# Performance work log

Measured on AMD Instinct MI355X. Metric: run time of the kernel, lower is better.

The kernel has to match this reference:

```python
import jax, jax.numpy as jnp
import numpy as np
from jax import lax

GRID_N = 80
C_FEAT = 128
HID = 256
NLAYERS = 12


def _make_grid_mesh(n):
    xs = np.linspace(-0.9, 0.9, n, dtype=np.float32)
    X, Y = np.meshgrid(xs, xs, indexing='xy')
    verts = np.stack([X.ravel(), Y.ravel(), np.zeros(n * n, np.float32)], 1)
    idx = np.arange(n * n).reshape(n, n)
    a = idx[:-1, :-1].ravel(); b = idx[:-1, 1:].ravel()
    c = idx[1:, :-1].ravel(); d = idx[1:, 1:].ravel()
    faces = np.concatenate([np.stack([a, b, c], 1), np.stack([b, d, c], 1)], 0)
    return verts, faces.astype(np.int64)


def _edges_and_inv(faces):
    F = faces.shape[0]
    e = np.concatenate([faces[:, [0, 1]], faces[:, [1, 2]], faces[:, [2, 0]]], 0)
    e = np.sort(e, 1)
    edges, inv = np.unique(e, axis=0, return_inverse=True)
    inv = inv.reshape(-1)
    return edges.astype(np.int32), inv[:F], inv[F:2 * F], inv[2 * F:]


def _subdivide_faces(faces, V):
    # new vertex k is midpoint of unique edge k, placed at index V + k
    edges, i01, i12, i20 = _edges_and_inv(faces)
    m01 = V + i01; m12 = V + i12; m20 = V + i20
    v0, v1, v2 = faces[:, 0], faces[:, 1], faces[:, 2]
    nf = np.concatenate([np.stack([v0, m01, m20], 1), np.stack([v1, m12, m01], 1),
                         np.stack([v2, m20, m12], 1), np.stack([m01, m12, m20], 1)], 0)
    return edges, nf


def _topology():
    verts0, f1 = _make_grid_mesh(GRID_N)
    V1 = verts0.shape[0]
    edges1, f2 = _subdivide_faces(f1, V1)
    V2 = V1 + edges1.shape[0]
    edges2, f3 = _subdivide_faces(f2, V2)
    V3 = V2 + edges2.shape[0]
    edges3 = _edges_and_inv(f3)[0]
    return verts0, edges1, edges2, edges3, V3


def _vert_align(feat, verts):
    # feat [C,H,W]; sample bilinearly at vertex (x,y) in [-1,1], align_corners, zero padding
    C, H, W = feat.shape
    fx = (verts[:, 0] + 1.0) * 0.5 * (W - 1)
    fy = (verts[:, 1] + 1.0) * 0.5 * (H - 1)
    x0 = jnp.floor(fx); y0 = jnp.floor(fy)
    wx = fx - x0; wy = fy - y0
    x0i = x0.astype(jnp.int32); y0i = y0.astype(jnp.int32)
    fT = jnp.transpose(feat, (1, 2, 0))  # [H,W,C]

    def samp(yi, xi):
        valid = ((yi >= 0) & (yi < H) & (xi >= 0) & (xi < W)).astype(feat.dtype)
        v = fT[jnp.clip(yi, 0, H - 1), jnp.clip(xi, 0, W - 1)]
        return v * valid[:, None]

    return (samp(y0i, x0i) * ((1 - wy) * (1 - wx))[:, None]
            + samp(y0i, x0i + 1) * ((1 - wy) * wx)[:, None]
            + samp(y0i + 1, x0i) * (wy * (1 - wx))[:, None]
            + samp(y0i + 1, x0i + 1) * (wy * wx)[:, None])


def _gconv(x, e0, e1, w, b):
    # pytorch3d GraphConv: w0(x) + sum_{j in N(i)} w1(x_j), undirected edges
    h0 = x @ w[0] + b[0]
    h1 = x @ w[1] + b[1]
    agg = jnp.zeros_like(h0).at[e0].add(h1[e1]).at[e1].add(h1[e0])
    return h0 + agg


def _stage(feat, edges, w_in, b_in, w_h, b_h, w_out, b_out):
    e0, e1 = edges[:, 0], edges[:, 1]
    x = _gconv(feat, e0, e1, w_in, b_in)

    def body(xc, p):
        return _gconv(xc, e0, e1, p[0], p[1]), None

    x, _ = lax.scan(body, x, (w_h, b_h))
    coords = _gconv(x, e0, e1, w_out, b_out)
    return x, coords


def _subdiv(f, edges):
    # SubdivideMeshes feature/vertex rule: append edge midpoints
    return jnp.concatenate([f, 0.5 * (f[edges[:, 0]] + f[edges[:, 1]])], 0)


def setup_inputs() -> dict:
    key = jax.random.key(0)
    ks = jax.random.split(key, 16)
    verts0, edges1, edges2, edges3, V3 = _topology()

    def pw(k, din, dout, L=None):
        shape = (L, 2, din, dout) if L else (2, din, dout)
        return jax.random.normal(k, shape, dtype=jnp.float32) / np.float32(np.sqrt(7.0 * din))

    din2 = C_FEAT + HID
    inp = {
        'conv64': jax.random.normal(ks[0], (C_FEAT, 56, 56), jnp.float32),
        'conv128': jax.random.normal(ks[1], (C_FEAT, 28, 28), jnp.float32),
        'conv256': jax.random.normal(ks[2], (C_FEAT, 14, 14), jnp.float32),
        'verts0': jnp.asarray(verts0),
        'edges1': jnp.asarray(edges1), 'edges2': jnp.asarray(edges2), 'edges3': jnp.asarray(edges3),
        'w_in1': pw(ks[3], C_FEAT, HID), 'b_in1': jnp.zeros((2, HID), jnp.float32),
        'w_h1': pw(ks[4], HID, HID, NLAYERS), 'b_h1': jnp.zeros((NLAYERS, 2, HID), jnp.float32),
        'w_out1': pw(ks[5], HID, 3), 'b_out1': jnp.zeros((2, 3), jnp.float32),
        'w_in2': pw(ks[6], din2, HID), 'b_in2': jnp.zeros((2, HID), jnp.float32),
        'w_h2': pw(ks[7], HID, HID, NLAYERS), 'b_h2': jnp.zeros((NLAYERS, 2, HID), jnp.float32),
        'w_out2': pw(ks[8], HID, 3), 'b_out2': jnp.zeros((2, 3), jnp.float32),
        'w_in3': pw(ks[9], din2, HID), 'b_in3': jnp.zeros((2, HID), jnp.float32),
        'w_h3': pw(ks[10], HID, HID, NLAYERS), 'b_h3': jnp.zeros((NLAYERS, 2, HID), jnp.float32),
        'w_out3': pw(ks[11], HID, 3), 'b_out3': jnp.zeros((2, 3), jnp.float32),
    }
    return inp


def reference(conv64, conv128, conv256, verts0,
              w_in1, b_in1, w_h1, b_h1, w_out1, b_out1,
              w_in2, b_in2, w_h2, b_h2, w_out2, b_out2,
              w_in3, b_in3, w_h3, b_h3, w_out3, b_out3,
              edges1, edges2, edges3):
    # stage 1: vert_align on conv64 + 14 graph convs -> coords
    x, c1 = _stage(_vert_align(conv64, verts0), edges1, w_in1, b_in1, w_h1, b_h1, w_out1, b_out1)
    v2 = _subdiv(c1, edges1)
    h2 = _subdiv(x, edges1)
    f2 = jnp.concatenate([_vert_align(conv128, v2), h2], 1)
    x, c2 = _stage(f2, edges2, w_in2, b_in2, w_h2, b_h2, w_out2, b_out2)
    v3 = _subdiv(c2, edges2)
    h3 = _subdiv(x, edges2)
    f3 = jnp.concatenate([_vert_align(conv256, v3), h3], 1)
    _, c3 = _stage(f3, edges3, w_in3, b_in3, w_h3, b_h3, w_out3, b_out3)
    return c3
```

## Files before the change

### kernel.cpp

```cpp
#include <hip/hip_runtime.h>
#include <utility>

#define HID 256

typedef __attribute__((ext_vector_type(8))) short bf16x8;
typedef __attribute__((ext_vector_type(4))) float f32x4;
typedef __attribute__((ext_vector_type(4))) unsigned short us4;
typedef __attribute__((ext_vector_type(8))) unsigned short us8;

constexpr size_t MAXN3 = 100489;
constexpr size_t MAXE3 = 300200;

constexpr size_t OFF_IN1 = 0;
constexpr size_t OFF_IN2 = OFF_IN1 + 2 * 256 * 128;
constexpr size_t OFF_IN3 = OFF_IN2 + 2 * 256 * 384;
constexpr size_t OFF_H1  = OFF_IN3 + 2 * 256 * 384;
constexpr size_t OFF_H2  = OFF_H1 + 24 * 256 * 256;
constexpr size_t OFF_H3  = OFF_H2 + 24 * 256 * 256;
constexpr size_t WT_TOTAL = OFF_H3 + 24 * 256 * 256;

__device__ __attribute__((aligned(16))) unsigned short g_Ah[MAXN3 * 256];
__device__ __attribute__((aligned(16))) unsigned short g_Al[MAXN3 * 256];
__device__ __attribute__((aligned(16))) unsigned short g_Bh[MAXN3 * 256];
__device__ __attribute__((aligned(16))) unsigned short g_Bl[MAXN3 * 256];
__device__ __attribute__((aligned(16))) unsigned short g_Gh[MAXN3 * 256];
__device__ __attribute__((aligned(16))) unsigned short g_Gl[MAXN3 * 256];
__device__ __attribute__((aligned(16))) unsigned short g_Dh[MAXN3 * 256];
__device__ __attribute__((aligned(16))) unsigned short g_Dl[MAXN3 * 256];
__device__ __attribute__((aligned(16))) unsigned short g_VAh[MAXN3 * 128];
__device__ __attribute__((aligned(16))) unsigned short g_VAl[MAXN3 * 128];
__device__ float g_C0[MAXN3 * 3];
__device__ float g_C2[MAXN3 * 3];
__device__ float g_Vv[MAXN3 * 3];
__device__ float g_T [56 * 56 * 128];
__device__ __attribute__((aligned(16))) unsigned short g_Wth[WT_TOTAL];
__device__ __attribute__((aligned(16))) unsigned short g_Wtl[WT_TOTAL];
__device__ int g_deg   [MAXN3];
__device__ int g_rowptr[MAXN3 + 1];
__device__ int g_cursor[MAXN3];
__device__ int g_adj   [2 * MAXE3];
__device__ int g_bsum  [128];

__device__ inline float b2f(unsigned short h) {
  return __uint_as_float((unsigned)h << 16);
}
__device__ inline void fsplit(float f, unsigned short& h, unsigned short& l) {
  unsigned u = __float_as_uint(f);
  h = (unsigned short)(u >> 16);
  float hf = __uint_as_float(u & 0xffff0000u);
  l = (unsigned short)(__float_as_uint(f - hf) >> 16);
}

#define GLOAD16(g, l)                                                       \
  __builtin_amdgcn_global_load_lds(                                        \
      (const __attribute__((address_space(1))) unsigned*)(const void*)(g), \
      (__attribute__((address_space(3))) unsigned*)(void*)(l), 16, 0, 0)

__global__ __launch_bounds__(256) void k_wtrans(const float* __restrict__ W,
                                                unsigned short* __restrict__ Oh,
                                                unsigned short* __restrict__ Ol,
                                                int K) {
  __shared__ float Ls[64][65];
  int ktb = blockIdx.x, cb = blockIdx.y, mat = blockIdx.z;
  int nktb = gridDim.x;
  const float* Wm = W + (size_t)mat * K * 256;
  int t = threadIdx.x;
#pragma unroll
  for (int i = 0; i < 16; ++i) {
    int idx = i * 256 + t;
    int kk = idx >> 6, cc = idx & 63;
    Ls[kk][cc] = Wm[(size_t)(ktb * 64 + kk) * 256 + cb * 64 + cc];
  }
  __syncthreads();
  size_t tb = ((size_t)(mat * 4 + cb) * nktb + ktb) * 4096;
#pragma unroll
  for (int i = 0; i < 2; ++i) {
    int c = t * 2 + i;
    int n = c >> 3, sp = c & 7;
    int kbase = (sp ^ (n & 7)) * 8;
    unsigned short hb[8], lb[8];
#pragma unroll
    for (int j = 0; j < 8; ++j) {
      float v = Ls[kbase + j][n];
      unsigned short hi, lo;
      fsplit(v, hi, lo);
      hb[j] = hi;
      lb[j] = lo;
    }
    *(us4*)(Oh + tb + c * 8)     = (us4){hb[0], hb[1], hb[2], hb[3]};
    *(us4*)(Oh + tb + c * 8 + 4) = (us4){hb[4], hb[5], hb[6], hb[7]};
    *(us4*)(Ol + tb + c * 8)     = (us4){lb[0], lb[1], lb[2], lb[3]};
    *(us4*)(Ol + tb + c * 8 + 4) = (us4){lb[4], lb[5], lb[6], lb[7]};
  }
}


__global__ __launch_bounds__(256) void k_count(const int* __restrict__ edges,
                                               int* __restrict__ deg, int E) {
  int e = blockIdx.x * blockDim.x + threadIdx.x;
  if (e >= E) return;
  atomicAdd(&deg[edges[2 * e + 0]], 1);
  atomicAdd(&deg[edges[2 * e + 1]], 1);
}

__global__ __launch_bounds__(256) void k_scan_part(const int* __restrict__ deg,
                                                   int* __restrict__ bsum, int N) {
  __shared__ int s[256];
  int t = threadIdx.x;
  int base = blockIdx.x * 1024 + t * 4;
  int v = 0;
#pragma unroll
  for (int i = 0; i < 4; ++i) {
    int idx = base + i;
    if (idx < N) v += deg[idx];
  }
  s[t] = v;
  __syncthreads();
  for (int off = 128; off > 0; off >>= 1) {
    if (t < off) s[t] += s[t + off];
    __syncthreads();
  }
  if (t == 0) bsum[blockIdx.x] = s[0];
}

__global__ __launch_bounds__(128) void k_scan_top(int* __restrict__ bsum, int nb) {
  __shared__ int s[128];
  int t = threadIdx.x;
  s[t] = (t < nb) ? bsum[t] : 0;
  __syncthreads();
  for (int off = 1; off < 128; off <<= 1) {
    int v = (t >= off) ? s[t - off] : 0;
    __syncthreads();
    s[t] += v;
    __syncthreads();
  }
  if (t < nb) bsum[t] = (t == 0) ? 0 : s[t - 1];
}

__global__ __launch_bounds__(256) void k_scan_write(const int* __restrict__ deg,
                                                    const int* __restrict__ bsum,
                                                    int* __restrict__ rowptr,
                                                    int* __restrict__ cursor, int N) {
  __shared__ int s[256];
  int t = threadIdx.x;
  int base = blockIdx.x * 1024;
  int d[4];
  int local = 0;
#pragma unroll
  for (int i = 0; i < 4; ++i) {
    int idx = base + t * 4 + i;
    d[i] = (idx < N) ? deg[idx] : 0;
    local += d[i];
  }
  s[t] = local;
  __syncthreads();
  for (int off = 1; off < 256; off <<= 1) {
    int v = (t >= off) ? s[t - off] : 0;
    __syncthreads();
    s[t] += v;
    __syncthreads();
  }
  int run = bsum[blockIdx.x] + s[t] - local;
#pragma unroll
  for (int i = 0; i < 4; ++i) {
    int idx = base + t * 4 + i;
    if (idx < N) {
      rowptr[idx] = run;
      cursor[idx] = run;
    }
    run += d[i];
  }
  if (blockIdx.x == gridDim.x - 1 && t == 255) rowptr[N] = run;
}

__global__ __launch_bounds__(256) void k_fill(const int* __restrict__ edges,
                                              int* __restrict__ cursor,
                                              int* __restrict__ adj, int E) {
  int e = blockIdx.x * blockDim.x + threadIdx.x;
  if (e >= E) return;
  int a = edges[2 * e + 0];
  int b = edges[2 * e + 1];
  adj[atomicAdd(&cursor[a], 1)] = b;
  adj[atomicAdd(&cursor[b], 1)] = a;
}


__global__ __launch_bounds__(128) void k_transpose(const float* __restrict__ in,
                                                   float* __restrict__ out, int HW) {
  int p = blockIdx.x;
  int c = threadIdx.x;
  if (p < HW) out[(size_t)p * 128 + c] = in[(size_t)c * HW + p];
}

__global__ __launch_bounds__(128) void k_vert_align(const float* __restrict__ fT,
                                                    const float* __restrict__ verts,
                                                    unsigned short* __restrict__ oh,
                                                    unsigned short* __restrict__ ol,
                                                    int N, int H, int W) {
  int v = blockIdx.x;
  if (v >= N) return;
  int c = threadIdx.x;
  float vx = verts[(size_t)v * 3 + 0];
  float vy = verts[(size_t)v * 3 + 1];
  float fx = (vx + 1.f) * 0.5f * (float)(W - 1);
  float fy = (vy + 1.f) * 0.5f * (float)(H - 1);
  float x0f = floorf(fx), y0f = floorf(fy);
  float wx = fx - x0f, wy = fy - y0f;
  int x0 = (int)x0f, y0 = (int)y0f;
  float acc = 0.f;
#pragma unroll
  for (int dy = 0; dy < 2; ++dy) {
#pragma unroll
    for (int dx = 0; dx < 2; ++dx) {
      int yi = y0 + dy, xi = x0 + dx;
      bool valid = (yi >= 0) && (yi < H) && (xi >= 0) && (xi < W);
      int yc = min(max(yi, 0), H - 1);
      int xc = min(max(xi, 0), W - 1);
      float val = fT[((size_t)yc * W + xc) * 128 + c];
      float wgt = (dy ? wy : 1.f - wy) * (dx ? wx : 1.f - wx);
      acc += valid ? val * wgt : 0.f;
    }
  }
  unsigned short h, l;
  fsplit(acc, h, l);
  oh[(size_t)v * 128 + c] = h;
  ol[(size_t)v * 128 + c] = l;
}

template <int CH>
__global__ __launch_bounds__(256) void k_gather(const int* __restrict__ rowptr,
                                                const int* __restrict__ adj,
                                                const unsigned short* __restrict__ Xh,
                                                const unsigned short* __restrict__ Xl,
                                                unsigned short* __restrict__ Gh,
                                                unsigned short* __restrict__ Gl, int N) {
  constexpr int TPV = CH / 8;
  int idx = blockIdx.x * blockDim.x + threadIdx.x;
  int v = idx / TPV;
  if (v >= N) return;
  int c = (idx % TPV) * 8;
  float a[8] = {};
  int lo = rowptr[v], hi = rowptr[v + 1];
  for (int i = lo; i < hi; ++i) {
    size_t base = (size_t)adj[i] * CH + c;
    us8 h = *(const us8*)(Xh + base);
    us8 l = *(const us8*)(Xl + base);
#pragma unroll
    for (int j = 0; j < 8; ++j) a[j] += b2f(h[j]) + b2f(l[j]);
  }
  us8 oh, ol;
#pragma unroll
  for (int j = 0; j < 8; ++j) {
    unsigned short hh, ll;
    fsplit(a[j], hh, ll);
    oh[j] = hh;
    ol[j] = ll;
  }
  *(us8*)(Gh + (size_t)v * CH + c) = oh;
  *(us8*)(Gl + (size_t)v * CH + c) = ol;
}

struct Panels {
  const unsigned short* ph[4];
  const unsigned short* pl[4];
  int ks[4];
  int ld[4];
};

#define SWZ(row, slot) (((row) * 64) + (((slot) ^ ((row) & 7)) << 3))

__global__ __launch_bounds__(256) void k_layer(
    Panels pd, int Kmm,
    const unsigned short* __restrict__ w0h, const unsigned short* __restrict__ w0l,
    const unsigned short* __restrict__ w1h, const unsigned short* __restrict__ w1l,
    int Kw,
    const float* __restrict__ b0, const float* __restrict__ b1,
    const int* __restrict__ deg,
    unsigned short* __restrict__ Yh, unsigned short* __restrict__ Yl, int N) {
  __shared__ __attribute__((aligned(16))) unsigned short Xh_lds[128 * 64];
  __shared__ __attribute__((aligned(16))) unsigned short Xl_lds[128 * 64];
  __shared__ __attribute__((aligned(16))) unsigned short Wh_lds[4096];
  __shared__ __attribute__((aligned(16))) unsigned short Wl_lds[4096];
  int tid = threadIdx.x;
  int lane = tid & 63;
  int wid = tid >> 6;
  int wm = wid & 1, wn = wid >> 1;

  int nrt = (N + 127) >> 7;
  int total = nrt * 4;
  int flat = blockIdx.x;
  int rowtile, colblk;
  if ((flat & ~31) + 32 <= total) {
    int sub = flat & 31;
    rowtile = (flat >> 5) * 8 + (sub & 7);
    colblk = sub >> 3;
  } else {
    rowtile = flat >> 2;
    colblk = flat & 3;
  }
  int row0 = rowtile * 128;
  int col0 = colblk * 64;
  int nktbw = Kw >> 6;

  f32x4 acc[4][2];
#pragma unroll
  for (int m = 0; m < 4; ++m)
#pragma unroll
    for (int n = 0; n < 2; ++n) acc[m][n] = (f32x4){0.f, 0.f, 0.f, 0.f};

  for (int kt = 0; kt < Kmm; kt += 64) {
    int pi = (kt >= pd.ks[1]) + (kt >= pd.ks[2]) + (kt >= pd.ks[3]);
    const unsigned short* bph = pd.ph[pi];
    const unsigned short* bpl = pd.pl[pi];
    int ld = pd.ld[pi];
    int koff = kt - pd.ks[pi];
#pragma unroll
    for (int i = 0; i < 4; ++i) {
      int c = (wid * 4 + i) * 64 + lane;
      int row = c >> 3, slot = c & 7;
      int vg = min(row0 + row, N - 1);
      size_t srcoff = (size_t)vg * ld + koff + ((slot ^ (row & 7)) << 3);
      GLOAD16(bph + srcoff, &Xh_lds[(size_t)c * 8]);
      GLOAD16(bpl + srcoff, &Xl_lds[(size_t)c * 8]);
    }
    const unsigned short* th;
    const unsigned short* tl;
    {
      int ktb = (kt < Kw) ? (kt >> 6) : ((kt - Kw) >> 6);
      const unsigned short* mh = (kt < Kw) ? w0h : w1h;
      const unsigned short* ml = (kt < Kw) ? w0l : w1l;
      size_t tb = ((size_t)(colblk * nktbw + ktb)) * 4096;
      th = mh + tb;
      tl = ml + tb;
    }
#pragma unroll
    for (int i = 0; i < 2; ++i) {
      int inst = wid * 2 + i;
      GLOAD16(th + inst * 512 + lane * 8, &Wh_lds[inst * 512]);
      GLOAD16(tl + inst * 512 + lane * 8, &Wl_lds[inst * 512]);
    }
    __syncthreads();
#pragma unroll
    for (int ks = 0; ks < 2; ++ks) {
      int slot = ks * 4 + (lane >> 4);
      bf16x8 ah[4], al[4];
#pragma unroll
      for (int m = 0; m < 4; ++m) {
        int row = wm * 64 + m * 16 + (lane & 15);
        int off = SWZ(row, slot);
        ah[m] = *(const bf16x8*)&Xh_lds[off];
        al[m] = *(const bf16x8*)&Xl_lds[off];
      }
      bf16x8 bh[2], bl[2];
#pragma unroll
      for (int n = 0; n < 2; ++n) {
        int nr = wn * 32 + n * 16 + (lane & 15);
        int wi = SWZ(nr, slot);
        bh[n] = *(const bf16x8*)&Wh_lds[wi];
        bl[n] = *(const bf16x8*)&Wl_lds[wi];
      }
#pragma unroll
      for (int m = 0; m < 4; ++m)
#pragma unroll
        for (int n = 0; n < 2; ++n) {
          f32x4 c = acc[m][n];
          c = __builtin_amdgcn_mfma_f32_16x16x32_bf16(al[m], bh[n], c, 0, 0, 0);
          c = __builtin_amdgcn_mfma_f32_16x16x32_bf16(ah[m], bl[n], c, 0, 0, 0);
          c = __builtin_amdgcn_mfma_f32_16x16x32_bf16(ah[m], bh[n], c, 0, 0, 0);
          acc[m][n] = c;
        }
    }
    __syncthreads();
  }

#pragma unroll
  for (int m = 0; m < 4; ++m) {
    int rbase = row0 + wm * 64 + m * 16 + (lane >> 4) * 4;
    float dv[4];
#pragma unroll
    for (int r = 0; r < 4; ++r)
      dv[r] = (rbase + r < N) ? (float)deg[rbase + r] : 0.f;
#pragma unroll
    for (int n = 0; n < 2; ++n) {
      int col = col0 + wn * 32 + n * 16 + (lane & 15);
      float bb0 = b0[col], bb1 = b1[col];
      f32x4 v = acc[m][n];
#pragma unroll
      for (int r = 0; r < 4; ++r) {
        int row = rbase + r;
        if (row < N) {
          unsigned short h, l;
          fsplit(v[r] + bb0 + dv[r] * bb1, h, l);
          Yh[(size_t)row * HID + col] = h;
          Yl[(size_t)row * HID + col] = l;
        }
      }
    }
  }
}

__global__ __launch_bounds__(256) void k_rowdot6(const unsigned short* __restrict__ Xh,
                                                 const unsigned short* __restrict__ Xl,
                                                 const float* __restrict__ W,
                                                 const float* __restrict__ b,
                                                 float* __restrict__ Y0,
                                                 float* __restrict__ Y1, int N) {
  int gid = blockIdx.x * blockDim.x + threadIdx.x;
  int row = gid >> 6;
  int lane = threadIdx.x & 63;
  if (row >= N) return;
  size_t base = (size_t)row * HID + lane * 4;
  us4 hv = *(const us4*)(Xh + base);
  us4 lv = *(const us4*)(Xl + base);
  float s[6] = {0.f, 0.f, 0.f, 0.f, 0.f, 0.f};
#pragma unroll
  for (int k = 0; k < 4; ++k) {
    float x = b2f(hv[k]) + b2f(lv[k]);
    int kk = lane * 4 + k;
#pragma unroll
    for (int j = 0; j < 3; ++j) {
      s[j]     += x * W[kk * 3 + j];
      s[3 + j] += x * W[768 + kk * 3 + j];
    }
  }
#pragma unroll
  for (int off = 32; off > 0; off >>= 1)
#pragma unroll
    for (int j = 0; j < 6; ++j) s[j] += __shfl_down(s[j], off);
  if (lane == 0) {
#pragma unroll
    for (int j = 0; j < 3; ++j) {
      Y0[(size_t)row * 3 + j] = s[j] + b[j];
      Y1[(size_t)row * 3 + j] = s[3 + j] + b[3 + j];
    }
  }
}

__global__ __launch_bounds__(256) void k_scatter3(const int* __restrict__ edges,
                                                  const float* __restrict__ H,
                                                  float* __restrict__ OUT, int E) {
  int e = blockIdx.x * blockDim.x + threadIdx.x;
  if (e >= E) return;
  int a = edges[(size_t)e * 2 + 0];
  int b = edges[(size_t)e * 2 + 1];
#pragma unroll
  for (int k = 0; k < 3; ++k) {
    atomicAdd(&OUT[(size_t)a * 3 + k], H[(size_t)b * 3 + k]);
    atomicAdd(&OUT[(size_t)b * 3 + k], H[(size_t)a * 3 + k]);
  }
}

__global__ __launch_bounds__(256) void k_subdiv3(const float* __restrict__ c,
                                                 const int* __restrict__ edges,
                                                 float* __restrict__ v, int N, int E) {
  int i = blockIdx.x * blockDim.x + threadIdx.x;
  if (i >= N + E) return;
  if (i < N) {
#pragma unroll
    for (int k = 0; k < 3; ++k) v[(size_t)i * 3 + k] = c[(size_t)i * 3 + k];
  } else {
    int e = i - N;
    int a = edges[(size_t)e * 2 + 0];
    int b = edges[(size_t)e * 2 + 1];
#pragma unroll
    for (int k = 0; k < 3; ++k)
      v[(size_t)i * 3 + k] = 0.5f * (c[(size_t)a * 3 + k] + c[(size_t)b * 3 + k]);
  }
}

__global__ __launch_bounds__(256) void k_subdiv_feat(const unsigned short* __restrict__ xh,
                                                     const unsigned short* __restrict__ xl,
                                                     const int* __restrict__ edges,
                                                     unsigned short* __restrict__ oh,
                                                     unsigned short* __restrict__ ol,
                                                     int N, int E) {
  int idx = blockIdx.x * blockDim.x + threadIdx.x;
  int v = idx >> 5;
  if (v >= N + E) return;
  int c = (idx & 31) * 8;
  us8 rh, rl;
  if (v < N) {
    rh = *(const us8*)(xh + (size_t)v * HID + c);
    rl = *(const us8*)(xl + (size_t)v * HID + c);
  } else {
    int e = v - N;
    int a = edges[(size_t)e * 2 + 0];
    int b = edges[(size_t)e * 2 + 1];
    us8 ahv = *(const us8*)(xh + (size_t)a * HID + c);
    us8 alv = *(const us8*)(xl + (size_t)a * HID + c);
    us8 bhv = *(const us8*)(xh + (size_t)b * HID + c);
    us8 blv = *(const us8*)(xl + (size_t)b * HID + c);
#pragma unroll
    for (int j = 0; j < 8; ++j) {
      float f = 0.5f * ((b2f(ahv[j]) + b2f(alv[j])) + (b2f(bhv[j]) + b2f(blv[j])));
      unsigned short hh, ll;
      fsplit(f, hh, ll);
      rh[j] = hh;
      rl[j] = ll;
    }
  }
  *(us8*)(oh + (size_t)v * HID + c) = rh;
  *(us8*)(ol + (size_t)v * HID + c) = rl;
}


extern "C" void kernel_launch(void* const* d_in, const int* in_sizes, int n_in,
                              void* d_out, int out_size, void* d_ws, size_t ws_size,
                              hipStream_t stream) {
  const float* conv64  = (const float*)d_in[0];
  const float* conv128 = (const float*)d_in[1];
  const float* conv256 = (const float*)d_in[2];
  const float* verts0  = (const float*)d_in[3];
  const int*   edges1  = (const int*)d_in[4];
  const int*   edges2  = (const int*)d_in[5];
  const int*   edges3  = (const int*)d_in[6];
  const float* w_in1 = (const float*)d_in[7],  *b_in1 = (const float*)d_in[8];
  const float* w_h1  = (const float*)d_in[9],  *b_h1  = (const float*)d_in[10];
  const float* w_out1= (const float*)d_in[11], *b_out1= (const float*)d_in[12];
  const float* w_in2 = (const float*)d_in[13], *b_in2 = (const float*)d_in[14];
  const float* w_h2  = (const float*)d_in[15], *b_h2  = (const float*)d_in[16];
  const float* w_out2= (const float*)d_in[17], *b_out2= (const float*)d_in[18];
  const float* w_in3 = (const float*)d_in[19], *b_in3 = (const float*)d_in[20];
  const float* w_h3  = (const float*)d_in[21], *b_h3  = (const float*)d_in[22];
  const float* w_out3= (const float*)d_in[23], *b_out3= (const float*)d_in[24];

  const int N1 = in_sizes[3] / 3;
  const int E1 = in_sizes[4] / 2;
  const int E2 = in_sizes[5] / 2;
  const int E3 = in_sizes[6] / 2;
  const int N2 = N1 + E1;
  const int N3 = N2 + E2;
  if ((size_t)N3 > MAXN3 || (size_t)E3 > MAXE3) return;

  unsigned short *Ah, *Al, *Bh, *Bl, *Gh, *Gl, *Dh, *Dl, *VAh, *VAl;
  float *C0, *C2, *Vv, *T;
  unsigned short *Wth, *Wtl;
  int *deg, *rowptr, *cursor, *adj, *bsum;
  hipGetSymbolAddress((void**)&Ah,  HIP_SYMBOL(g_Ah));
  hipGetSymbolAddress((void**)&Al,  HIP_SYMBOL(g_Al));
  hipGetSymbolAddress((void**)&Bh,  HIP_SYMBOL(g_Bh));
  hipGetSymbolAddress((void**)&Bl,  HIP_SYMBOL(g_Bl));
  hipGetSymbolAddress((void**)&Gh,  HIP_SYMBOL(g_Gh));
  hipGetSymbolAddress((void**)&Gl,  HIP_SYMBOL(g_Gl));
  hipGetSymbolAddress((void**)&Dh,  HIP_SYMBOL(g_Dh));
  hipGetSymbolAddress((void**)&Dl,  HIP_SYMBOL(g_Dl));
  hipGetSymbolAddress((void**)&VAh, HIP_SYMBOL(g_VAh));
  hipGetSymbolAddress((void**)&VAl, HIP_SYMBOL(g_VAl));
  hipGetSymbolAddress((void**)&C0, HIP_SYMBOL(g_C0));
  hipGetSymbolAddress((void**)&C2, HIP_SYMBOL(g_C2));
  hipGetSymbolAddress((void**)&Vv, HIP_SYMBOL(g_Vv));
  hipGetSymbolAddress((void**)&T,  HIP_SYMBOL(g_T));
  hipGetSymbolAddress((void**)&Wth, HIP_SYMBOL(g_Wth));
  hipGetSymbolAddress((void**)&Wtl, HIP_SYMBOL(g_Wtl));
  hipGetSymbolAddress((void**)&deg,    HIP_SYMBOL(g_deg));
  hipGetSymbolAddress((void**)&rowptr, HIP_SYMBOL(g_rowptr));
  hipGetSymbolAddress((void**)&cursor, HIP_SYMBOL(g_cursor));
  hipGetSymbolAddress((void**)&adj,    HIP_SYMBOL(g_adj));
  hipGetSymbolAddress((void**)&bsum,   HIP_SYMBOL(g_bsum));

  k_wtrans<<<dim3(2, 4, 2),  256, 0, stream>>>(w_in1, Wth + OFF_IN1, Wtl + OFF_IN1, 128);
  k_wtrans<<<dim3(6, 4, 2),  256, 0, stream>>>(w_in2, Wth + OFF_IN2, Wtl + OFF_IN2, 384);
  k_wtrans<<<dim3(6, 4, 2),  256, 0, stream>>>(w_in3, Wth + OFF_IN3, Wtl + OFF_IN3, 384);
  k_wtrans<<<dim3(4, 4, 24), 256, 0, stream>>>(w_h1,  Wth + OFF_H1,  Wtl + OFF_H1,  256);
  k_wtrans<<<dim3(4, 4, 24), 256, 0, stream>>>(w_h2,  Wth + OFF_H2,  Wtl + OFF_H2,  256);
  k_wtrans<<<dim3(4, 4, 24), 256, 0, stream>>>(w_h3,  Wth + OFF_H3,  Wtl + OFF_H3,  256);

  const int BIG = 0x7fffffff;

  auto layerGrid = [](int N) { return dim3((unsigned)(((N + 127) / 128) * 4)); };

  auto build_csr = [&](const int* edges, int E, int N) {
    hipMemsetAsync(deg, 0, (size_t)N * sizeof(int), stream);
    k_count<<<(E + 255) / 256, 256, 0, stream>>>(edges, deg, E);
    int nb = (N + 1023) / 1024;
    k_scan_part<<<nb, 256, 0, stream>>>(deg, bsum, N);
    k_scan_top<<<1, 128, 0, stream>>>(bsum, nb);
    k_scan_write<<<nb, 256, 0, stream>>>(deg, bsum, rowptr, cursor, N);
    k_fill<<<(E + 255) / 256, 256, 0, stream>>>(edges, cursor, adj, E);
  };

  auto gconv_hidden = [&](size_t offH, const float* bh, int N) {
    unsigned short *Xh = Ah, *Xl = Al, *Yh = Bh, *Yl = Bl;
    for (int l = 0; l < 12; ++l) {
      const unsigned short* w0h = Wth + offH + (size_t)(2 * l + 0) * 65536;
      const unsigned short* w0l = Wtl + offH + (size_t)(2 * l + 0) * 65536;
      const unsigned short* w1h = Wth + offH + (size_t)(2 * l + 1) * 65536;
      const unsigned short* w1l = Wtl + offH + (size_t)(2 * l + 1) * 65536;
      const float* b0 = bh + (size_t)l * 2 * HID;
      const float* b1 = b0 + HID;
      k_gather<256><<<((size_t)N * 32 + 255) / 256, 256, 0, stream>>>(
          rowptr, adj, Xh, Xl, Gh, Gl, N);
      Panels pd = {{Xh, Gh, nullptr, nullptr}, {Xl, Gl, nullptr, nullptr},
                   {0, 256, BIG, BIG}, {256, 256, 0, 0}};
      k_layer<<<layerGrid(N), 256, 0, stream>>>(pd, 512, w0h, w0l, w1h, w1l, 256,
                                                b0, b1, deg, Yh, Yl, N);
      std::swap(Xh, Yh);
      std::swap(Xl, Yl);
    }
  };

  auto gconv_out = [&](const unsigned short* Xh, const unsigned short* Xl,
                       const float* wo, const float* bo,
                       float* Cdst, const int* edges, int E, int N) {
    k_rowdot6<<<((size_t)N * 64 + 255) / 256, 256, 0, stream>>>(Xh, Xl, wo, bo, Cdst, C2, N);
    k_scatter3<<<(E + 255) / 256, 256, 0, stream>>>(edges, C2, Cdst, E);
  };

  build_csr(edges1, E1, N1);
  k_transpose<<<56 * 56, 128, 0, stream>>>(conv64, T, 56 * 56);
  k_vert_align<<<N1, 128, 0, stream>>>(T, verts0, VAh, VAl, N1, 56, 56);
  k_gather<128><<<((size_t)N1 * 16 + 255) / 256, 256, 0, stream>>>(
      rowptr, adj, VAh, VAl, Gh, Gl, N1);
  {
    Panels pd = {{VAh, Gh, nullptr, nullptr}, {VAl, Gl, nullptr, nullptr},
                 {0, 128, BIG, BIG}, {128, 128, 0, 0}};
    k_layer<<<layerGrid(N1), 256, 0, stream>>>(pd, 256,
        Wth + OFF_IN1, Wtl + OFF_IN1, Wth + OFF_IN1 + 32768, Wtl + OFF_IN1 + 32768, 128,
        b_in1, b_in1 + HID, deg, Ah, Al, N1);
  }
  gconv_hidden(OFF_H1, b_h1, N1);
  gconv_out(Ah, Al, w_out1, b_out1, C0, edges1, E1, N1);
  k_subdiv3<<<(N2 + 255) / 256, 256, 0, stream>>>(C0, edges1, Vv, N1, E1);
  k_subdiv_feat<<<((size_t)N2 * 32 + 255) / 256, 256, 0, stream>>>(
      Ah, Al, edges1, Dh, Dl, N1, E1);

  build_csr(edges2, E2, N2);
  k_transpose<<<28 * 28, 128, 0, stream>>>(conv128, T, 28 * 28);
  k_vert_align<<<N2, 128, 0, stream>>>(T, Vv, VAh, VAl, N2, 28, 28);
  k_gather<128><<<((size_t)N2 * 16 + 255) / 256, 256, 0, stream>>>(
      rowptr, adj, VAh, VAl, Gh, Gl, N2);
  k_gather<256><<<((size_t)N2 * 32 + 255) / 256, 256, 0, stream>>>(
      rowptr, adj, Dh, Dl, Bh, Bl, N2);
  {
    const size_t m0 = OFF_IN2, m1 = OFF_IN2 + (size_t)256 * 384;
    Panels pd = {{VAh, Dh, Gh, Bh}, {VAl, Dl, Gl, Bl},
                 {0, 128, 384, 512}, {128, 256, 128, 256}};
    k_layer<<<layerGrid(N2), 256, 0, stream>>>(pd, 768,
        Wth + m0, Wtl + m0, Wth + m1, Wtl + m1, 384,
        b_in2, b_in2 + HID, deg, Ah, Al, N2);
  }
  gconv_hidden(OFF_H2, b_h2, N2);
  gconv_out(Ah, Al, w_out2, b_out2, C0, edges2, E2, N2);
  k_subdiv3<<<(N3 + 255) / 256, 256, 0, stream>>>(C0, edges2, Vv, N2, E2);
  k_subdiv_feat<<<((size_t)N3 * 32 + 255) / 256, 256, 0, stream>>>(
      Ah, Al, edges2, Dh, Dl, N2, E2);

  build_csr(edges3, E3, N3);
  k_transpose<<<14 * 14, 128, 0, stream>>>(conv256, T, 14 * 14);
  k_vert_align<<<N3, 128, 0, stream>>>(T, Vv, VAh, VAl, N3, 14, 14);
  k_gather<128><<<((size_t)N3 * 16 + 255) / 256, 256, 0, stream>>>(
      rowptr, adj, VAh, VAl, Gh, Gl, N3);
  k_gather<256><<<((size_t)N3 * 32 + 255) / 256, 256, 0, stream>>>(
      rowptr, adj, Dh, Dl, Bh, Bl, N3);
  {
    const size_t m0 = OFF_IN3, m1 = OFF_IN3 + (size_t)256 * 384;
    Panels pd = {{VAh, Dh, Gh, Bh}, {VAl, Dl, Gl, Bl},
                 {0, 128, 384, 512}, {128, 256, 128, 256}};
    k_layer<<<layerGrid(N3), 256, 0, stream>>>(pd, 768,
        Wth + m0, Wtl + m0, Wth + m1, Wtl + m1, 384,
        b_in3, b_in3 + HID, deg, Ah, Al, N3);
  }
  gconv_hidden(OFF_H3, b_h3, N3);
  float* OUT = (float*)d_out;
  k_rowdot6<<<((size_t)N3 * 64 + 255) / 256, 256, 0, stream>>>(
      Ah, Al, w_out3, b_out3, OUT, C2, N3);
  k_scatter3<<<(E3 + 255) / 256, 256, 0, stream>>>(edges3, C2, OUT, E3);
}
```

Measured before the change: 4.221 ms.

## Double-buffer LDS tiles and widen layer GEMM tile to 128x128 with 8 waves

The layer GEMM kernel now uses 512 threads per block computing a 128x128 output tile instead of 128x64. This halves the grid and halves re-reads of the activation panel. The K loop is software-pipelined with double-buffered LDS, so the next tile's global-to-LDS loads are issued before computing the current one, and one barrier per iteration is removed. LDS use roughly quadruples to about 96KB per block, which may limit blocks per CU, and launch_bounds(512,2) tightens the register budget.

```diff
diff --git a/kernel.cpp b/kernel.cpp
--- a/kernel.cpp
+++ b/kernel.cpp
@@ -269,7 +269,7 @@
 
 #define SWZ(row, slot) (((row) * 64) + (((slot) ^ ((row) & 7)) << 3))
 
-__global__ __launch_bounds__(256) void k_layer(
+__global__ __launch_bounds__(512, 2) void k_layer(
     Panels pd, int Kmm,
     const unsigned short* __restrict__ w0h, const unsigned short* __restrict__ w0l,
     const unsigned short* __restrict__ w1h, const unsigned short* __restrict__ w1l,
@@ -277,29 +277,30 @@
     const float* __restrict__ b0, const float* __restrict__ b1,
     const int* __restrict__ deg,
     unsigned short* __restrict__ Yh, unsigned short* __restrict__ Yl, int N) {
-  __shared__ __attribute__((aligned(16))) unsigned short Xh_lds[128 * 64];
-  __shared__ __attribute__((aligned(16))) unsigned short Xl_lds[128 * 64];
-  __shared__ __attribute__((aligned(16))) unsigned short Wh_lds[4096];
-  __shared__ __attribute__((aligned(16))) unsigned short Wl_lds[4096];
+  __shared__ __attribute__((aligned(16))) unsigned short Xh_lds[2][128 * 64];
+  __shared__ __attribute__((aligned(16))) unsigned short Xl_lds[2][128 * 64];
+  __shared__ __attribute__((aligned(16))) unsigned short Wh_lds[2][2 * 4096];
+  __shared__ __attribute__((aligned(16))) unsigned short Wl_lds[2][2 * 4096];
   int tid = threadIdx.x;
   int lane = tid & 63;
   int wid = tid >> 6;
-  int wm = wid & 1, wn = wid >> 1;
+  int wm = wid >> 2;
+  int wn = wid & 3;
 
   int nrt = (N + 127) >> 7;
-  int total = nrt * 4;
+  int total = nrt * 2;
   int flat = blockIdx.x;
   int rowtile, colblk;
-  if ((flat & ~31) + 32 <= total) {
-    int sub = flat & 31;
-    rowtile = (flat >> 5) * 8 + (sub & 7);
+  if ((flat & ~15) + 16 <= total) {
+    int sub = flat & 15;
+    rowtile = (flat >> 4) * 8 + (sub & 7);
     colblk = sub >> 3;
   } else {
-    rowtile = flat >> 2;
-    colblk = flat & 3;
+    rowtile = flat >> 1;
+    colblk = flat & 1;
   }
   int row0 = rowtile * 128;
-  int col0 = colblk * 64;
+  int col0 = colblk * 128;
   int nktbw = Kw >> 6;
 
   f32x4 acc[4][2];
@@ -308,38 +309,35 @@
 #pragma unroll
     for (int n = 0; n < 2; ++n) acc[m][n] = (f32x4){0.f, 0.f, 0.f, 0.f};
 
-  for (int kt = 0; kt < Kmm; kt += 64) {
+  auto STAGE = [&](int buf, int kt) {
     int pi = (kt >= pd.ks[1]) + (kt >= pd.ks[2]) + (kt >= pd.ks[3]);
     const unsigned short* bph = pd.ph[pi];
     const unsigned short* bpl = pd.pl[pi];
     int ld = pd.ld[pi];
     int koff = kt - pd.ks[pi];
 #pragma unroll
-    for (int i = 0; i < 4; ++i) {
-      int c = (wid * 4 + i) * 64 + lane;
+    for (int i = 0; i < 2; ++i) {
+      int c = tid + i * 512;
       int row = c >> 3, slot = c & 7;
       int vg = min(row0 + row, N - 1);
-      size_t srcoff = (size_t)vg * ld + koff + ((slot ^ (row & 7)) << 3);
-      GLOAD16(bph + srcoff, &Xh_lds[(size_t)c * 8]);
-      GLOAD16(bpl + srcoff, &Xl_lds[(size_t)c * 8]);
-    }
-    const unsigned short* th;
-    const unsigned short* tl;
-    {
-      int ktb = (kt < Kw) ? (kt >> 6) : ((kt - Kw) >> 6);
-      const unsigned short* mh = (kt < Kw) ? w0h : w1h;
-      const unsigned short* ml = (kt < Kw) ? w0l : w1l;
-      size_t tb = ((size_t)(colblk * nktbw + ktb)) * 4096;
-      th = mh + tb;
-      tl = ml + tb;
-    }
+      size_t so = (size_t)vg * ld + koff + ((slot ^ (row & 7)) << 3);
+      GLOAD16(bph + so, &Xh_lds[buf][(size_t)c * 8]);
+      GLOAD16(bpl + so, &Xl_lds[buf][(size_t)c * 8]);
+    }
+    int ktb = (kt < Kw) ? (kt >> 6) : ((kt - Kw) >> 6);
+    const unsigned short* mh = (kt < Kw) ? w0h : w1h;
+    const unsigned short* ml = (kt < Kw) ? w0l : w1l;
 #pragma unroll
     for (int i = 0; i < 2; ++i) {
-      int inst = wid * 2 + i;
-      GLOAD16(th + inst * 512 + lane * 8, &Wh_lds[inst * 512]);
-      GLOAD16(tl + inst * 512 + lane * 8, &Wl_lds[inst * 512]);
-    }
-    __syncthreads();
+      int c = tid + i * 512;
+      int half = c >> 9, ci = c & 511;
+      size_t tb = ((size_t)((2 * colblk + half) * nktbw + ktb)) * 4096 + (size_t)ci * 8;
+      GLOAD16(mh + tb, &Wh_lds[buf][half * 4096 + ci * 8]);
+      GLOAD16(ml + tb, &Wl_lds[buf][half * 4096 + ci * 8]);
+    }
+  };
+
+  auto COMPUTE = [&](int buf) {
 #pragma unroll
     for (int ks = 0; ks < 2; ++ks) {
       int slot = ks * 4 + (lane >> 4);
@@ -348,16 +346,16 @@
       for (int m = 0; m < 4; ++m) {
         int row = wm * 64 + m * 16 + (lane & 15);
         int off = SWZ(row, slot);
-        ah[m] = *(const bf16x8*)&Xh_lds[off];
-        al[m] = *(const bf16x8*)&Xl_lds[off];
+        ah[m] = *(const bf16x8*)&Xh_lds[buf][off];
+        al[m] = *(const bf16x8*)&Xl_lds[buf][off];
       }
       bf16x8 bh[2], bl[2];
 #pragma unroll
       for (int n = 0; n < 2; ++n) {
         int nr = wn * 32 + n * 16 + (lane & 15);
-        int wi = SWZ(nr, slot);
-        bh[n] = *(const bf16x8*)&Wh_lds[wi];
-        bl[n] = *(const bf16x8*)&Wl_lds[wi];
+        int off = (nr >> 6) * 4096 + SWZ(nr & 63, slot);
+        bh[n] = *(const bf16x8*)&Wh_lds[buf][off];
+        bl[n] = *(const bf16x8*)&Wl_lds[buf][off];
       }
 #pragma unroll
       for (int m = 0; m < 4; ++m)
@@ -370,7 +368,17 @@
           acc[m][n] = c;
         }
     }
+  };
+
+  int nt = Kmm >> 6;
+  STAGE(0, 0);
+  __syncthreads();
+  int buf = 0;
+  for (int t = 0; t < nt; ++t) {
+    if (t + 1 < nt) STAGE(buf ^ 1, (t + 1) << 6);
+    COMPUTE(buf);
     __syncthreads();
+    buf ^= 1;
   }
 
 #pragma unroll
@@ -567,7 +575,7 @@
 
   const int BIG = 0x7fffffff;
 
-  auto layerGrid = [](int N) { return dim3((unsigned)(((N + 127) / 128) * 4)); };
+  auto layerGrid = [](int N) { return dim3((unsigned)(((N + 127) / 128) * 2)); };
 
   auto build_csr = [&](const int* edges, int E, int N) {
     hipMemsetAsync(deg, 0, (size_t)N * sizeof(int), stream);
@@ -592,7 +600,7 @@
           rowptr, adj, Xh, Xl, Gh, Gl, N);
       Panels pd = {{Xh, Gh, nullptr, nullptr}, {Xl, Gl, nullptr, nullptr},
                    {0, 256, BIG, BIG}, {256, 256, 0, 0}};
-      k_layer<<<layerGrid(N), 256, 0, stream>>>(pd, 512, w0h, w0l, w1h, w1l, 256,
+      k_layer<<<layerGrid(N), 512, 0, stream>>>(pd, 512, w0h, w0l, w1h, w1l, 256,
                                                 b0, b1, deg, Yh, Yl, N);
       std::swap(Xh, Yh);
       std::swap(Xl, Yl);
@@ -614,7 +622,7 @@
   {
     Panels pd = {{VAh, Gh, nullptr, nullptr}, {VAl, Gl, nullptr, nullptr},
                  {0, 128, BIG, BIG}, {128, 128, 0, 0}};
-    k_layer<<<layerGrid(N1), 256, 0, stream>>>(pd, 256,
+    k_layer<<<layerGrid(N1), 512, 0, stream>>>(pd, 256,
         Wth + OFF_IN1, Wtl + OFF_IN1, Wth + OFF_IN1 + 32768, Wtl + OFF_IN1 + 32768, 128,
         b_in1, b_in1 + HID, deg, Ah, Al, N1);
   }
@@ -635,7 +643,7 @@
     const size_t m0 = OFF_IN2, m1 = OFF_IN2 + (size_t)256 * 384;
     Panels pd = {{VAh, Dh, Gh, Bh}, {VAl, Dl, Gl, Bl},
                  {0, 128, 384, 512}, {128, 256, 128, 256}};
-    k_layer<<<layerGrid(N2), 256, 0, stream>>>(pd, 768,
+    k_layer<<<layerGrid(N2), 512, 0, stream>>>(pd, 768,
         Wth + m0, Wtl + m0, Wth + m1, Wtl + m1, 384,
         b_in2, b_in2 + HID, deg, Ah, Al, N2);
   }
@@ -656,7 +664,7 @@
     const size_t m0 = OFF_IN3, m1 = OFF_IN3 + (size_t)256 * 384;
     Panels pd = {{VAh, Dh, Gh, Bh}, {VAl, Dl, Gl, Bl},
                  {0, 128, 384, 512}, {128, 256, 128, 256}};
-    k_layer<<<layerGrid(N3), 256, 0, stream>>>(pd, 768,
+    k_layer<<<layerGrid(N3), 512, 0, stream>>>(pd, 768,
         Wth + m0, Wtl + m0, Wth + m1, Wtl + m1, 384,
         b_in3, b_in3 + HID, deg, Ah, Al, N3);
   }
```

Result: slower. 4.377 ms (+3.7%).

## Widen layer GEMM output tile to 128 columns to halve X panel reloads

Applied to the files above, without the earlier changes.

Each block of the layer GEMM now computes a 128x128 output tile instead of 128x64. Each wave covers 64x64 with a 4x4 MFMA accumulator array, and the grid is halved. This halves how often the activation panels (high and low bf16 halves) are reloaded from global memory per column block, and raises MFMA work per LDS load. In exchange it doubles weight LDS and accumulator registers, with launch bounds asking for 2 blocks per CU, and on smaller meshes it gives fewer blocks.

```diff
diff --git a/kernel.cpp b/kernel.cpp
--- a/kernel.cpp
+++ b/kernel.cpp
@@ -269,7 +269,7 @@
 
 #define SWZ(row, slot) (((row) * 64) + (((slot) ^ ((row) & 7)) << 3))
 
-__global__ __launch_bounds__(256) void k_layer(
+__global__ __launch_bounds__(256, 2) void k_layer(
     Panels pd, int Kmm,
     const unsigned short* __restrict__ w0h, const unsigned short* __restrict__ w0l,
     const unsigned short* __restrict__ w1h, const unsigned short* __restrict__ w1l,
@@ -279,34 +279,35 @@
     unsigned short* __restrict__ Yh, unsigned short* __restrict__ Yl, int N) {
   __shared__ __attribute__((aligned(16))) unsigned short Xh_lds[128 * 64];
   __shared__ __attribute__((aligned(16))) unsigned short Xl_lds[128 * 64];
-  __shared__ __attribute__((aligned(16))) unsigned short Wh_lds[4096];
-  __shared__ __attribute__((aligned(16))) unsigned short Wl_lds[4096];
+  __shared__ __attribute__((aligned(16))) unsigned short Wh_lds[2 * 4096];
+  __shared__ __attribute__((aligned(16))) unsigned short Wl_lds[2 * 4096];
   int tid = threadIdx.x;
   int lane = tid & 63;
   int wid = tid >> 6;
-  int wm = wid & 1, wn = wid >> 1;
+  int wm = wid >> 1;
+  int wn = wid & 1;
 
   int nrt = (N + 127) >> 7;
-  int total = nrt * 4;
+  int total = nrt * 2;
   int flat = blockIdx.x;
   int rowtile, colblk;
-  if ((flat & ~31) + 32 <= total) {
-    int sub = flat & 31;
-    rowtile = (flat >> 5) * 8 + (sub & 7);
+  if ((flat & ~15) + 16 <= total) {
+    int sub = flat & 15;
+    rowtile = (flat >> 4) * 8 + (sub & 7);
     colblk = sub >> 3;
   } else {
-    rowtile = flat >> 2;
-    colblk = flat & 3;
+    rowtile = flat >> 1;
+    colblk = flat & 1;
   }
   int row0 = rowtile * 128;
-  int col0 = colblk * 64;
+  int col0 = colblk * 128;
   int nktbw = Kw >> 6;
 
-  f32x4 acc[4][2];
+  f32x4 acc[4][4];
 #pragma unroll
   for (int m = 0; m < 4; ++m)
 #pragma unroll
-    for (int n = 0; n < 2; ++n) acc[m][n] = (f32x4){0.f, 0.f, 0.f, 0.f};
+    for (int n = 0; n < 4; ++n) acc[m][n] = (f32x4){0.f, 0.f, 0.f, 0.f};
 
   for (int kt = 0; kt < Kmm; kt += 64) {
     int pi = (kt >= pd.ks[1]) + (kt >= pd.ks[2]) + (kt >= pd.ks[3]);
@@ -319,25 +320,22 @@
       int c = (wid * 4 + i) * 64 + lane;
       int row = c >> 3, slot = c & 7;
       int vg = min(row0 + row, N - 1);
-      size_t srcoff = (size_t)vg * ld + koff + ((slot ^ (row & 7)) << 3);
-      GLOAD16(bph + srcoff, &Xh_lds[(size_t)c * 8]);
-      GLOAD16(bpl + srcoff, &Xl_lds[(size_t)c * 8]);
-    }
-    const unsigned short* th;
-    const unsigned short* tl;
+      size_t so = (size_t)vg * ld + koff + ((slot ^ (row & 7)) << 3);
+      GLOAD16(bph + so, &Xh_lds[(size_t)c * 8]);
+      GLOAD16(bpl + so, &Xl_lds[(size_t)c * 8]);
+    }
     {
       int ktb = (kt < Kw) ? (kt >> 6) : ((kt - Kw) >> 6);
       const unsigned short* mh = (kt < Kw) ? w0h : w1h;
       const unsigned short* ml = (kt < Kw) ? w0l : w1l;
-      size_t tb = ((size_t)(colblk * nktbw + ktb)) * 4096;
-      th = mh + tb;
-      tl = ml + tb;
-    }
-#pragma unroll
-    for (int i = 0; i < 2; ++i) {
-      int inst = wid * 2 + i;
-      GLOAD16(th + inst * 512 + lane * 8, &Wh_lds[inst * 512]);
-      GLOAD16(tl + inst * 512 + lane * 8, &Wl_lds[inst * 512]);
+#pragma unroll
+      for (int i = 0; i < 4; ++i) {
+        int c = (wid * 4 + i) * 64 + lane;
+        int half = c >> 9, ci = c & 511;
+        size_t tb = ((size_t)((2 * colblk + half) * nktbw + ktb)) * 4096 + (size_t)ci * 8;
+        GLOAD16(mh + tb, &Wh_lds[half * 4096 + ci * 8]);
+        GLOAD16(ml + tb, &Wl_lds[half * 4096 + ci * 8]);
+      }
     }
     __syncthreads();
 #pragma unroll
@@ -351,18 +349,18 @@
         ah[m] = *(const bf16x8*)&Xh_lds[off];
         al[m] = *(const bf16x8*)&Xl_lds[off];
       }
-      bf16x8 bh[2], bl[2];
-#pragma unroll
-      for (int n = 0; n < 2; ++n) {
-        int nr = wn * 32 + n * 16 + (lane & 15);
-        int wi = SWZ(nr, slot);
-        bh[n] = *(const bf16x8*)&Wh_lds[wi];
-        bl[n] = *(const bf16x8*)&Wl_lds[wi];
+      bf16x8 bh[4], bl[4];
+#pragma unroll
+      for (int n = 0; n < 4; ++n) {
+        int nr = n * 16 + (lane & 15);
+        int off = wn * 4096 + SWZ(nr, slot);
+        bh[n] = *(const bf16x8*)&Wh_lds[off];
+        bl[n] = *(const bf16x8*)&Wl_lds[off];
       }
 #pragma unroll
       for (int m = 0; m < 4; ++m)
 #pragma unroll
-        for (int n = 0; n < 2; ++n) {
+        for (int n = 0; n < 4; ++n) {
           f32x4 c = acc[m][n];
           c = __builtin_amdgcn_mfma_f32_16x16x32_bf16(al[m], bh[n], c, 0, 0, 0);
           c = __builtin_amdgcn_mfma_f32_16x16x32_bf16(ah[m], bl[n], c, 0, 0, 0);
@@ -381,8 +379,8 @@
     for (int r = 0; r < 4; ++r)
       dv[r] = (rbase + r < N) ? (float)deg[rbase + r] : 0.f;
 #pragma unroll
-    for (int n = 0; n < 2; ++n) {
-      int col = col0 + wn * 32 + n * 16 + (lane & 15);
+    for (int n = 0; n < 4; ++n) {
+      int col = col0 + wn * 64 + n * 16 + (lane & 15);
       float bb0 = b0[col], bb1 = b1[col];
       f32x4 v = acc[m][n];
 #pragma unroll
@@ -567,7 +565,7 @@
 
   const int BIG = 0x7fffffff;
 
-  auto layerGrid = [](int N) { return dim3((unsigned)(((N + 127) / 128) * 4)); };
+  auto layerGrid = [](int N) { return dim3((unsigned)(((N + 127) / 128) * 2)); };
 
   auto build_csr = [&](const int* edges, int E, int N) {
     hipMemsetAsync(deg, 0, (size_t)N * sizeof(int), stream);
```

New measurement: 4.070 ms. 1.04x faster.
